# Performance work log

Hardware: AMD Instinct MI355X
Metric: run time of the kernel (lower is better)

The kernel has to match this reference:

```python
import jax, jax.numpy as jnp
import numpy as np

ALPHA = 300.0   # attractor_alpha
N_ATT = 16      # n_attractors
MIN_D = 0.001
MAX_D = 10.0


def _resize_bilinear_ac(x, out_h, out_w):
    """Bilinear resize with align_corners=True on trailing (H, W) dims of [B,C,h,w]."""
    h, w = x.shape[-2], x.shape[-1]
    ys = jnp.arange(out_h, dtype=jnp.float32) * ((h - 1) / max(out_h - 1, 1))
    xs = jnp.arange(out_w, dtype=jnp.float32) * ((w - 1) / max(out_w - 1, 1))
    y0 = jnp.floor(ys).astype(jnp.int32); y1 = jnp.minimum(y0 + 1, h - 1)
    x0 = jnp.floor(xs).astype(jnp.int32); x1 = jnp.minimum(x0 + 1, w - 1)
    wy = (ys - y0.astype(jnp.float32))[:, None]   # [out_h, 1]
    wx = (xs - x0.astype(jnp.float32))[None, :]   # [1, out_w]
    v00 = x[..., y0[:, None], x0[None, :]]
    v01 = x[..., y0[:, None], x1[None, :]]
    v10 = x[..., y1[:, None], x0[None, :]]
    v11 = x[..., y1[:, None], x1[None, :]]
    top = v00 * (1 - wx) + v01 * wx
    bot = v10 * (1 - wx) + v11 * wx
    return top * (1 - wy) + bot * wy


def setup_inputs() -> dict:
    key = jax.random.key(0)
    k = jax.random.split(key, 7)
    B, C, H, W = 4, 128, 192, 192
    n_bins = 64
    x = jax.random.normal(k[0], (B, C, H, W), dtype=jnp.float32)
    prev_bin = jax.random.uniform(k[1], (B, n_bins, H // 2, W // 2), dtype=jnp.float32)
    prev_bin_embedding = jax.random.normal(k[2], (B, C, H // 2, W // 2), dtype=jnp.float32)
    w1 = jax.random.normal(k[3], (128, 128), dtype=jnp.float32) * 0.05
    b1 = jnp.zeros((128,), dtype=jnp.float32)
    w2 = jax.random.normal(k[4], (2 * N_ATT, 128), dtype=jnp.float32) * 0.05
    b2 = jnp.zeros((2 * N_ATT,), dtype=jnp.float32)
    return {"x": x, "prev_bin": prev_bin, "prev_bin_embedding": prev_bin_embedding,
            "w1": w1, "b1": b1, "w2": w2, "b2": b2}


def reference(x, prev_bin, prev_bin_embedding, w1, b1, w2, b2):
    B, C, H, W = x.shape
    # add (interpolated) previous bin embedding
    pe = _resize_bilinear_ac(prev_bin_embedding, H, W)
    h = x + pe
    # per-pixel MLP (two 1x1 convs)
    h = jax.nn.relu(jnp.einsum('bchw,oc->bohw', h, w1) + b1[:, None, None])
    att = jax.nn.relu(jnp.einsum('bchw,oc->bohw', h, w2) + b2[:, None, None]) + 0.001
    # [B, n_attractors, 2, H, W] -> take normed attractor points
    att = att.reshape(B, N_ATT, 2, H, W)[:, :, 0]          # [B, nA, H, W]
    # upsample previous bin centers to feature resolution
    bc = _resize_bilinear_ac(prev_bin, H, W)               # [B, nB, H, W]
    # broadcast-subtract + inverse attractor + mean over attractors
    dx = att[:, :, None, :, :] - bc[:, None, :, :, :]      # [B, nA, nB, H, W]
    delta_c = jnp.mean(dx / (1.0 + ALPHA * dx * dx), axis=1)  # gamma = 2
    bin_new_centers = bc + delta_c
    bin_centers = (MAX_D - MIN_D) * bin_new_centers + MIN_D
    bin_centers = jnp.clip(jnp.sort(bin_centers, axis=1), MIN_D, MAX_D)
    return bin_new_centers, bin_centers
```

## Files before the change

### kernel.cpp

```cpp
#include <hip/hip_runtime.h>

constexpr int Bc = 4, Cc = 128, Hc = 192, Wc = 192;
constexpr int HI = 96, WI = 96;
constexpr int NB = 64;
constexpr int NA = 16;
constexpr float SCL = 95.0f / 191.0f;

typedef __attribute__((ext_vector_type(8))) short bf16x8;
typedef __attribute__((ext_vector_type(4))) float f32x4;

__device__ __forceinline__ unsigned short f2bf(float f) {
  unsigned u = __builtin_bit_cast(unsigned, f);
  unsigned r = (u + 0x7FFFu + ((u >> 16) & 1u)) >> 16;
  return (unsigned short)r;
}

__device__ __forceinline__ float rcp_fast(float r) {
#if defined(__has_builtin)
#if __has_builtin(__builtin_amdgcn_rcpf)
  return __builtin_amdgcn_rcpf(r);
#else
  return 1.0f / r;
#endif
#else
  return 1.0f / r;
#endif
}

__global__ __launch_bounds__(256) void k_prep(
    const float* __restrict__ w1, const float* __restrict__ w2,
    unsigned short* __restrict__ w1bf, unsigned short* __restrict__ w2bf)
{
  const int t = blockIdx.x * 256 + threadIdx.x;
  if (t < 16384) {
    w1bf[t] = f2bf(w1[t]);
  } else {
    const int u = t - 16384;
    const int j = u >> 7, c = u & 127;
    w2bf[u] = f2bf(w2[(2 * j) * 128 + c]);
  }
}

__global__ __launch_bounds__(256) void k_att(
    const float* __restrict__ x, const float* __restrict__ pbe,
    const unsigned short* __restrict__ w1bf, const float* __restrict__ b1,
    const unsigned short* __restrict__ w2bf, const float* __restrict__ b2,
    float* __restrict__ att)
{
  constexpr int PH = 136;
  __shared__ __align__(16) unsigned char smem[64 * PH * 2 + 128 * 36 * 4];
  unsigned short* h_s  = (unsigned short*)smem;
  float*          row_s = (float*)(smem + 64 * PH * 2);
  unsigned short* a1_s = (unsigned short*)(smem + 64 * PH * 2);

  const int tid = threadIdx.x;
  const int xg0 = blockIdx.x * 64;
  const int y = blockIdx.y;
  const int b = blockIdx.z;

  const float ysf = y * SCL;
  const int y0 = (int)ysf;
  const int y1 = min(y0 + 1, HI - 1);
  const float wy = ysf - (float)y0;
  const int xi0 = (int)(xg0 * SCL);

  #pragma unroll
  for (int i = 0; i < 18; ++i) {
    const int f = tid + 256 * i;
    const int c = f / 36;
    const int xi = f - c * 36;
    const int xgl = min(xi0 + xi, WI - 1);
    const float* p = pbe + (size_t)(b * Cc + c) * (HI * WI);
    const float top = p[y0 * WI + xgl];
    const float bot = p[y1 * WI + xgl];
    row_s[c * 36 + xi] = top + wy * (bot - top);
  }
  __syncthreads();

  #pragma unroll
  for (int i = 0; i < 8; ++i) {
    const int f4 = tid + 256 * i;
    const int c = f4 >> 4;
    const int q = f4 & 15;
    const float4 xv = *(const float4*)&x[((size_t)(b * Cc + c) * Hc + y) * Wc + xg0 + 4 * q];
    const float xa[4] = {xv.x, xv.y, xv.z, xv.w};
    #pragma unroll
    for (int r = 0; r < 4; ++r) {
      const int px = 4 * q + r;
      const float xsf = (float)(xg0 + px) * SCL;
      const int x0 = (int)xsf;
      const float wx = xsf - (float)x0;
      const int xl = x0 - xi0;
      const float v0 = row_s[c * 36 + xl];
      const float v1 = row_s[c * 36 + xl + 1];
      h_s[px * PH + c] = f2bf(xa[r] + v0 + wx * (v1 - v0));
    }
  }
  __syncthreads();

  const int lane = tid & 63;
  const int wv = tid >> 6;
  const int ln = lane & 15;
  const int qd = lane >> 4;
  const int m0 = wv * 16;

  bf16x8 af[4];
  #pragma unroll
  for (int kt = 0; kt < 4; ++kt)
    af[kt] = *(const bf16x8*)&h_s[(m0 + ln) * PH + kt * 32 + qd * 8];

  f32x4 acc[8];
  #pragma unroll
  for (int nt = 0; nt < 8; ++nt) acc[nt] = f32x4{0.f, 0.f, 0.f, 0.f};

  #pragma unroll
  for (int nt = 0; nt < 8; ++nt) {
    #pragma unroll
    for (int kt = 0; kt < 4; ++kt) {
      const bf16x8 bf = *(const bf16x8*)&w1bf[(nt * 16 + ln) * 128 + kt * 32 + qd * 8];
      acc[nt] = __builtin_amdgcn_mfma_f32_16x16x32_bf16(af[kt], bf, acc[nt], 0, 0, 0);
    }
  }

  #pragma unroll
  for (int nt = 0; nt < 8; ++nt) {
    const int n = nt * 16 + ln;
    const float bias = b1[n];
    #pragma unroll
    for (int r = 0; r < 4; ++r) {
      const int m = m0 + qd * 4 + r;
      a1_s[m * PH + n] = f2bf(fmaxf(acc[nt][r] + bias, 0.f));
    }
  }

  f32x4 acc2 = f32x4{0.f, 0.f, 0.f, 0.f};
  #pragma unroll
  for (int kt = 0; kt < 4; ++kt) {
    const bf16x8 a2 = *(const bf16x8*)&a1_s[(m0 + ln) * PH + kt * 32 + qd * 8];
    const bf16x8 b2f = *(const bf16x8*)&w2bf[ln * 128 + kt * 32 + qd * 8];
    acc2 = __builtin_amdgcn_mfma_f32_16x16x32_bf16(a2, b2f, acc2, 0, 0, 0);
  }
  const float bias2 = b2[2 * ln];
  #pragma unroll
  for (int r = 0; r < 4; ++r) {
    const int px = m0 + qd * 4 + r;
    const float v = fmaxf(acc2[r] + bias2, 0.f) + 0.001f;
    att[((size_t)((b * Hc + y) * Wc) + xg0 + px) * NA + ln] = v;
  }
}

__global__ __launch_bounds__(192) void k_bins(
    const float* __restrict__ pb, const float* __restrict__ att,
    float* __restrict__ out0, float* __restrict__ out1)
{
  __shared__ __align__(16) float pbs[NB][2][WI];

  const int tid = threadIdx.x;
  const int y = blockIdx.x;
  const int b = blockIdx.y;

  const float ysf = y * SCL;
  const int y0 = (int)ysf;
  const int y1 = min(y0 + 1, HI - 1);
  const float wy = ysf - (float)y0;

  #pragma unroll
  for (int i = 0; i < 16; ++i) {
    const int u = tid + 192 * i;
    const int k = u / 48;
    const int rem = u - k * 48;
    const int r = rem / 24;
    const int xi4 = rem - r * 24;
    const int yr = r ? y1 : y0;
    const float4 v = *(const float4*)&pb[(size_t)(b * NB + k) * (HI * WI) + yr * WI + xi4 * 4];
    *(float4*)&pbs[k][r][xi4 * 4] = v;
  }

  float am[16];
  {
    const float4* ap = (const float4*)(att + ((size_t)((b * Hc + y) * Wc) + tid) * NA);
    const float4 a0 = ap[0], a1 = ap[1], a2 = ap[2], a3 = ap[3];
    am[0] = a0.x;  am[1] = a0.y;  am[2] = a0.z;  am[3] = a0.w;
    am[4] = a1.x;  am[5] = a1.y;  am[6] = a1.z;  am[7] = a1.w;
    am[8] = a2.x;  am[9] = a2.y;  am[10] = a2.z; am[11] = a2.w;
    am[12] = a3.x; am[13] = a3.y; am[14] = a3.z; am[15] = a3.w;
  }
  __syncthreads();

  const float xsf = tid * SCL;
  const int x0 = (int)xsf;
  const float wx = xsf - (float)x0;

  const size_t obase = (size_t)(b * NB) * (Hc * Wc) + (size_t)y * Wc + tid;
  float v[NB];

  #pragma unroll
  for (int k = 0; k < NB; ++k) {
    const float v00 = pbs[k][0][x0], v01 = pbs[k][0][x0 + 1];
    const float v10 = pbs[k][1][x0], v11 = pbs[k][1][x0 + 1];
    const float top = v00 + wx * (v01 - v00);
    const float bot = v10 + wx * (v11 - v10);
    const float bc = top + wy * (bot - top);
    float delta = 0.f;
    #pragma unroll
    for (int j = 0; j < NA; ++j) {
      const float d = am[j] - bc;
      const float rq = fmaf(300.f * d, d, 1.f);
      delta = fmaf(d, rcp_fast(rq), delta);
    }
    const float bnc = fmaf(delta, 1.f / 16.f, bc);
    out0[obase + (size_t)k * (Hc * Wc)] = bnc;
    v[k] = fmaf(9.999f, bnc, 0.001f);
  }

  #pragma unroll
  for (int size = 2; size <= NB; size <<= 1) {
    #pragma unroll
    for (int stride = size >> 1; stride >= 1; stride >>= 1) {
      #pragma unroll
      for (int i = 0; i < NB; ++i) {
        if ((i & stride) == 0) {
          const int j = i | stride;
          const bool asc = ((i & size) == 0);
          const float a = v[i], c = v[j];
          const float lo = fminf(a, c), hi = fmaxf(a, c);
          v[i] = asc ? lo : hi;
          v[j] = asc ? hi : lo;
        }
      }
    }
  }

  #pragma unroll
  for (int k = 0; k < NB; ++k) {
    out1[obase + (size_t)k * (Hc * Wc)] = fminf(fmaxf(v[k], 0.001f), 10.0f);
  }
}

extern "C" void kernel_launch(void* const* d_in, const int* in_sizes, int n_in,
                              void* d_out, int out_size, void* d_ws, size_t ws_size,
                              hipStream_t stream) {
  const float* x   = (const float*)d_in[0];
  const float* pb  = (const float*)d_in[1];
  const float* pbe = (const float*)d_in[2];
  const float* w1  = (const float*)d_in[3];
  const float* b1  = (const float*)d_in[4];
  const float* w2  = (const float*)d_in[5];
  const float* b2  = (const float*)d_in[6];

  float* out0 = (float*)d_out;
  float* out1 = out0 + (size_t)Bc * NB * Hc * Wc;

  unsigned short* w1bf = (unsigned short*)d_ws;
  unsigned short* w2bf = w1bf + 16384;
  float* att = (float*)((char*)d_ws + 65536);

  k_prep<<<72, 256, 0, stream>>>(w1, w2, w1bf, w2bf);

  dim3 g1(Wc / 64, Hc, Bc);
  k_att<<<g1, 256, 0, stream>>>(x, pbe, w1bf, b1, w2bf, b2, att);

  dim3 g2(Hc, Bc);
  k_bins<<<g2, 192, 0, stream>>>(pb, att, out0, out1);
}
```

Baseline: 242.6 us.

## Fuse attractor MLP and bin-center update into one kernel with split bitonic sort

Merges the attractor MLP kernel and the bin-update/sort kernel into a single kernel. Attractor values now stay in shared memory instead of making a round trip through a global workspace. The prev_bin rows are prefetched into registers while the MFMAs run. The 64-element per-pixel sort is split across two threads, each sorting 32 values, followed by a merge step through shared memory. This cuts register pressure and drops one launch, at the cost of more shared memory, extra barriers, and idle threads during the sort.

After: 264.7 us. 1.09x slower.

```diff
diff --git a/kernel.cpp b/kernel.cpp
--- a/kernel.cpp
+++ b/kernel.cpp
@@ -41,17 +41,21 @@
   }
 }
 
-__global__ __launch_bounds__(256) void k_att(
+__global__ __launch_bounds__(256) void k_fused(
     const float* __restrict__ x, const float* __restrict__ pbe,
+    const float* __restrict__ pb,
     const unsigned short* __restrict__ w1bf, const float* __restrict__ b1,
     const unsigned short* __restrict__ w2bf, const float* __restrict__ b2,
-    float* __restrict__ att)
+    float* __restrict__ out0, float* __restrict__ out1)
 {
   constexpr int PH = 136;
-  __shared__ __align__(16) unsigned char smem[64 * PH * 2 + 128 * 36 * 4];
-  unsigned short* h_s  = (unsigned short*)smem;
-  float*          row_s = (float*)(smem + 64 * PH * 2);
-  unsigned short* a1_s = (unsigned short*)(smem + 64 * PH * 2);
+  __shared__ __align__(16) unsigned char smem[40000];
+  unsigned short* h_s   = (unsigned short*)smem;
+  float*          pbs   = (float*)smem;
+  float*          row_s = (float*)(smem + 17408);
+  unsigned short* a1_s  = (unsigned short*)(smem + 17408);
+  float*          srt   = (float*)(smem + 17408);
+  float*          att_s = (float*)(smem + 35840);
 
   const int tid = threadIdx.x;
   const int xg0 = blockIdx.x * 64;
@@ -108,11 +112,24 @@
   #pragma unroll
   for (int kt = 0; kt < 4; ++kt)
     af[kt] = *(const bf16x8*)&h_s[(m0 + ln) * PH + kt * 32 + qd * 8];
+  __syncthreads();
+
+  float pbv[17];
+  #pragma unroll
+  for (int i = 0; i < 17; ++i) {
+    const int u = tid + 256 * i;
+    const int k = u / 68;
+    const int rem = u - k * 68;
+    const int r = (rem >= 34) ? 1 : 0;
+    const int xi = rem - 34 * r;
+    const int xgl = min(xi0 + xi, WI - 1);
+    const int yr = r ? y1 : y0;
+    pbv[i] = pb[(size_t)(b * NB + k) * (HI * WI) + yr * WI + xgl];
+  }
 
   f32x4 acc[8];
   #pragma unroll
   for (int nt = 0; nt < 8; ++nt) acc[nt] = f32x4{0.f, 0.f, 0.f, 0.f};
-
   #pragma unroll
   for (int nt = 0; nt < 8; ++nt) {
     #pragma unroll
@@ -140,100 +157,107 @@
     const bf16x8 b2f = *(const bf16x8*)&w2bf[ln * 128 + kt * 32 + qd * 8];
     acc2 = __builtin_amdgcn_mfma_f32_16x16x32_bf16(a2, b2f, acc2, 0, 0, 0);
   }
-  const float bias2 = b2[2 * ln];
-  #pragma unroll
-  for (int r = 0; r < 4; ++r) {
-    const int px = m0 + qd * 4 + r;
-    const float v = fmaxf(acc2[r] + bias2, 0.f) + 0.001f;
-    att[((size_t)((b * Hc + y) * Wc) + xg0 + px) * NA + ln] = v;
-  }
-}
-
-__global__ __launch_bounds__(192) void k_bins(
-    const float* __restrict__ pb, const float* __restrict__ att,
-    float* __restrict__ out0, float* __restrict__ out1)
-{
-  __shared__ __align__(16) float pbs[NB][2][WI];
-
-  const int tid = threadIdx.x;
-  const int y = blockIdx.x;
-  const int b = blockIdx.y;
-
-  const float ysf = y * SCL;
-  const int y0 = (int)ysf;
-  const int y1 = min(y0 + 1, HI - 1);
-  const float wy = ysf - (float)y0;
-
-  #pragma unroll
-  for (int i = 0; i < 16; ++i) {
-    const int u = tid + 192 * i;
-    const int k = u / 48;
-    const int rem = u - k * 48;
-    const int r = rem / 24;
-    const int xi4 = rem - r * 24;
-    const int yr = r ? y1 : y0;
-    const float4 v = *(const float4*)&pb[(size_t)(b * NB + k) * (HI * WI) + yr * WI + xi4 * 4];
-    *(float4*)&pbs[k][r][xi4 * 4] = v;
-  }
-
-  float am[16];
   {
-    const float4* ap = (const float4*)(att + ((size_t)((b * Hc + y) * Wc) + tid) * NA);
-    const float4 a0 = ap[0], a1 = ap[1], a2 = ap[2], a3 = ap[3];
-    am[0] = a0.x;  am[1] = a0.y;  am[2] = a0.z;  am[3] = a0.w;
-    am[4] = a1.x;  am[5] = a1.y;  am[6] = a1.z;  am[7] = a1.w;
-    am[8] = a2.x;  am[9] = a2.y;  am[10] = a2.z; am[11] = a2.w;
-    am[12] = a3.x; am[13] = a3.y; am[14] = a3.z; am[15] = a3.w;
-  }
-  __syncthreads();
-
-  const float xsf = tid * SCL;
-  const int x0 = (int)xsf;
-  const float wx = xsf - (float)x0;
-
-  const size_t obase = (size_t)(b * NB) * (Hc * Wc) + (size_t)y * Wc + tid;
-  float v[NB];
-
-  #pragma unroll
-  for (int k = 0; k < NB; ++k) {
-    const float v00 = pbs[k][0][x0], v01 = pbs[k][0][x0 + 1];
-    const float v10 = pbs[k][1][x0], v11 = pbs[k][1][x0 + 1];
-    const float top = v00 + wx * (v01 - v00);
-    const float bot = v10 + wx * (v11 - v10);
-    const float bc = top + wy * (bot - top);
-    float delta = 0.f;
-    #pragma unroll
-    for (int j = 0; j < NA; ++j) {
-      const float d = am[j] - bc;
-      const float rq = fmaf(300.f * d, d, 1.f);
-      delta = fmaf(d, rcp_fast(rq), delta);
-    }
-    const float bnc = fmaf(delta, 1.f / 16.f, bc);
-    out0[obase + (size_t)k * (Hc * Wc)] = bnc;
-    v[k] = fmaf(9.999f, bnc, 0.001f);
-  }
-
-  #pragma unroll
-  for (int size = 2; size <= NB; size <<= 1) {
-    #pragma unroll
-    for (int stride = size >> 1; stride >= 1; stride >>= 1) {
+    const float bias2 = b2[2 * ln];
+    #pragma unroll
+    for (int r = 0; r < 4; ++r) {
+      const int px = m0 + qd * 4 + r;
+      att_s[ln * 65 + px] = fmaxf(acc2[r] + bias2, 0.f) + 0.001f;
+    }
+  }
+
+  #pragma unroll
+  for (int i = 0; i < 17; ++i)
+    pbs[tid + 256 * i] = pbv[i];
+  __syncthreads();
+
+  const int px = tid & 63;
+  const int xg = xg0 + px;
+  {
+    const float xsf = xg * SCL;
+    const int x0 = (int)xsf;
+    const float wx = xsf - (float)x0;
+    const int xl = x0 - xi0;
+
+    float am[16];
+    #pragma unroll
+    for (int j = 0; j < NA; ++j) am[j] = att_s[j * 65 + px];
+
+    const size_t obase = (size_t)(b * NB) * (Hc * Wc) + (size_t)y * Wc + xg;
+    #pragma unroll
+    for (int i = 0; i < 16; ++i) {
+      const int k = wv * 16 + i;
+      const float v00 = pbs[k * 68 + xl],      v01 = pbs[k * 68 + xl + 1];
+      const float v10 = pbs[k * 68 + 34 + xl], v11 = pbs[k * 68 + 34 + xl + 1];
+      const float top = v00 + wx * (v01 - v00);
+      const float bot = v10 + wx * (v11 - v10);
+      const float bc = top + wy * (bot - top);
+      float delta = 0.f;
       #pragma unroll
-      for (int i = 0; i < NB; ++i) {
+      for (int j = 0; j < NA; ++j) {
+        const float d = am[j] - bc;
+        const float rq = fmaf(300.f * d, d, 1.f);
+        delta = fmaf(d, rcp_fast(rq), delta);
+      }
+      const float bnc = fmaf(delta, 1.f / 16.f, bc);
+      out0[obase + (size_t)k * (Hc * Wc)] = bnc;
+      srt[k * 64 + px] = fmaf(9.999f, bnc, 0.001f);
+    }
+  }
+  __syncthreads();
+
+  float sv[32];
+  const int half = tid >> 6;
+  if (tid < 128) {
+    #pragma unroll
+    for (int i = 0; i < 32; ++i) sv[i] = srt[(half * 32 + i) * 64 + px];
+    const bool desc = (half == 1);
+    #pragma unroll
+    for (int size = 2; size <= 32; size <<= 1) {
+      #pragma unroll
+      for (int stride = size >> 1; stride >= 1; stride >>= 1) {
+        #pragma unroll
+        for (int i = 0; i < 32; ++i) {
+          if ((i & stride) == 0) {
+            const int j = i | stride;
+            const bool up = (((i & size) == 0) != desc);
+            const float a = sv[i], c = sv[j];
+            const float lo = fminf(a, c), hi = fmaxf(a, c);
+            sv[i] = up ? lo : hi;
+            sv[j] = up ? hi : lo;
+          }
+        }
+      }
+    }
+    #pragma unroll
+    for (int i = 0; i < 32; ++i) srt[(half * 32 + i) * 64 + px] = sv[i];
+  }
+  __syncthreads();
+
+  if (tid < 128) {
+    #pragma unroll
+    for (int i = 0; i < 32; ++i) {
+      const float partner = srt[((1 - half) * 32 + i) * 64 + px];
+      sv[i] = half ? fmaxf(sv[i], partner) : fminf(sv[i], partner);
+    }
+    #pragma unroll
+    for (int stride = 16; stride >= 1; stride >>= 1) {
+      #pragma unroll
+      for (int i = 0; i < 32; ++i) {
         if ((i & stride) == 0) {
           const int j = i | stride;
-          const bool asc = ((i & size) == 0);
-          const float a = v[i], c = v[j];
-          const float lo = fminf(a, c), hi = fmaxf(a, c);
-          v[i] = asc ? lo : hi;
-          v[j] = asc ? hi : lo;
+          const float a = sv[i], c = sv[j];
+          sv[i] = fminf(a, c);
+          sv[j] = fmaxf(a, c);
         }
       }
     }
-  }
-
-  #pragma unroll
-  for (int k = 0; k < NB; ++k) {
-    out1[obase + (size_t)k * (Hc * Wc)] = fminf(fmaxf(v[k], 0.001f), 10.0f);
+    const size_t obase = (size_t)(b * NB) * (Hc * Wc) + (size_t)y * Wc + xg0 + px;
+    #pragma unroll
+    for (int i = 0; i < 32; ++i) {
+      const int k = half * 32 + i;
+      out1[obase + (size_t)k * (Hc * Wc)] = fminf(fmaxf(sv[i], 0.001f), 10.0f);
+    }
   }
 }
 
@@ -253,13 +277,9 @@
 
   unsigned short* w1bf = (unsigned short*)d_ws;
   unsigned short* w2bf = w1bf + 16384;
-  float* att = (float*)((char*)d_ws + 65536);
 
   k_prep<<<72, 256, 0, stream>>>(w1, w2, w1bf, w2bf);
 
-  dim3 g1(Wc / 64, Hc, Bc);
-  k_att<<<g1, 256, 0, stream>>>(x, pbe, w1bf, b1, w2bf, b2, att);
-
-  dim3 g2(Hc, Bc);
-  k_bins<<<g2, 192, 0, stream>>>(pb, att, out0, out1);
-}
+  dim3 grid(Wc / 64, Hc, Bc);
+  k_fused<<<grid, 256, 0, stream>>>(x, pbe, pb, w1bf, b1, w2bf, b2, out0, out1);
+}
```

## Fuse x load and horizontal interp into MFMA fragment build, shrink LDS

Applied to the files above, without the earlier changes.

k_att no longer stages the interpolated activations in a separate LDS tile. Each lane now reads x straight from global memory and interpolates from a bf16 row buffer while building its MFMA A fragments, which drops one LDS round trip and one barrier and shrinks LDS to allow more resident blocks. The cost is uncoalesced scalar global loads of x (one pixel per lane across channels) and bf16 rounding of the interpolated embedding. k_bins interleaves four bins per attractor loop for ILP, and both kernels get occupancy hints in launch_bounds.

New measurement: 242.5 us. No clear change (-0.0%).

```diff
diff --git a/kernel.cpp b/kernel.cpp
--- a/kernel.cpp
+++ b/kernel.cpp
@@ -14,7 +14,10 @@
   unsigned r = (u + 0x7FFFu + ((u >> 16) & 1u)) >> 16;
   return (unsigned short)r;
 }
-
+__device__ __forceinline__ float bf2f(unsigned short h) {
+  unsigned u = ((unsigned)h) << 16;
+  return __builtin_bit_cast(float, u);
+}
 __device__ __forceinline__ float rcp_fast(float r) {
 #if defined(__has_builtin)
 #if __has_builtin(__builtin_amdgcn_rcpf)
@@ -41,17 +44,16 @@
   }
 }
 
-__global__ __launch_bounds__(256) void k_att(
+__global__ __launch_bounds__(256, 4) void k_att(
     const float* __restrict__ x, const float* __restrict__ pbe,
     const unsigned short* __restrict__ w1bf, const float* __restrict__ b1,
     const unsigned short* __restrict__ w2bf, const float* __restrict__ b2,
     float* __restrict__ att)
 {
   constexpr int PH = 136;
-  __shared__ __align__(16) unsigned char smem[64 * PH * 2 + 128 * 36 * 4];
-  unsigned short* h_s  = (unsigned short*)smem;
-  float*          row_s = (float*)(smem + 64 * PH * 2);
-  unsigned short* a1_s = (unsigned short*)(smem + 64 * PH * 2);
+  __shared__ __align__(16) unsigned char smem[64 * PH * 2];
+  unsigned short* rowb = (unsigned short*)smem;
+  unsigned short* a1_s = (unsigned short*)smem;
 
   const int tid = threadIdx.x;
   const int xg0 = blockIdx.x * 64;
@@ -73,28 +75,7 @@
     const float* p = pbe + (size_t)(b * Cc + c) * (HI * WI);
     const float top = p[y0 * WI + xgl];
     const float bot = p[y1 * WI + xgl];
-    row_s[c * 36 + xi] = top + wy * (bot - top);
-  }
-  __syncthreads();
-
-  #pragma unroll
-  for (int i = 0; i < 8; ++i) {
-    const int f4 = tid + 256 * i;
-    const int c = f4 >> 4;
-    const int q = f4 & 15;
-    const float4 xv = *(const float4*)&x[((size_t)(b * Cc + c) * Hc + y) * Wc + xg0 + 4 * q];
-    const float xa[4] = {xv.x, xv.y, xv.z, xv.w};
-    #pragma unroll
-    for (int r = 0; r < 4; ++r) {
-      const int px = 4 * q + r;
-      const float xsf = (float)(xg0 + px) * SCL;
-      const int x0 = (int)xsf;
-      const float wx = xsf - (float)x0;
-      const int xl = x0 - xi0;
-      const float v0 = row_s[c * 36 + xl];
-      const float v1 = row_s[c * 36 + xl + 1];
-      h_s[px * PH + c] = f2bf(xa[r] + v0 + wx * (v1 - v0));
-    }
+    rowb[c * 36 + xi] = f2bf(top + wy * (bot - top));
   }
   __syncthreads();
 
@@ -104,15 +85,30 @@
   const int qd = lane >> 4;
   const int m0 = wv * 16;
 
+  const int px = m0 + ln;
+  const int xg = xg0 + px;
+  const float xsf = (float)xg * SCL;
+  const int x0i = (int)xsf;
+  const float wx = xsf - (float)x0i;
+  const int xl = x0i - xi0;
+
   bf16x8 af[4];
   #pragma unroll
-  for (int kt = 0; kt < 4; ++kt)
-    af[kt] = *(const bf16x8*)&h_s[(m0 + ln) * PH + kt * 32 + qd * 8];
+  for (int kt = 0; kt < 4; ++kt) {
+    #pragma unroll
+    for (int j = 0; j < 8; ++j) {
+      const int c = kt * 32 + qd * 8 + j;
+      const float xv = x[((size_t)(b * Cc + c) * Hc + y) * Wc + xg];
+      const float v0 = bf2f(rowb[c * 36 + xl]);
+      const float v1 = bf2f(rowb[c * 36 + xl + 1]);
+      af[kt][j] = (short)f2bf(xv + v0 + wx * (v1 - v0));
+    }
+  }
+  __syncthreads();
 
   f32x4 acc[8];
   #pragma unroll
   for (int nt = 0; nt < 8; ++nt) acc[nt] = f32x4{0.f, 0.f, 0.f, 0.f};
-
   #pragma unroll
   for (int nt = 0; nt < 8; ++nt) {
     #pragma unroll
@@ -143,13 +139,13 @@
   const float bias2 = b2[2 * ln];
   #pragma unroll
   for (int r = 0; r < 4; ++r) {
-    const int px = m0 + qd * 4 + r;
+    const int opx = m0 + qd * 4 + r;
     const float v = fmaxf(acc2[r] + bias2, 0.f) + 0.001f;
-    att[((size_t)((b * Hc + y) * Wc) + xg0 + px) * NA + ln] = v;
-  }
-}
-
-__global__ __launch_bounds__(192) void k_bins(
+    att[((size_t)((b * Hc + y) * Wc) + xg0 + opx) * NA + ln] = v;
+  }
+}
+
+__global__ __launch_bounds__(192, 2) void k_bins(
     const float* __restrict__ pb, const float* __restrict__ att,
     float* __restrict__ out0, float* __restrict__ out1)
 {
@@ -195,22 +191,34 @@
   float v[NB];
 
   #pragma unroll
-  for (int k = 0; k < NB; ++k) {
-    const float v00 = pbs[k][0][x0], v01 = pbs[k][0][x0 + 1];
-    const float v10 = pbs[k][1][x0], v11 = pbs[k][1][x0 + 1];
-    const float top = v00 + wx * (v01 - v00);
-    const float bot = v10 + wx * (v11 - v10);
-    const float bc = top + wy * (bot - top);
-    float delta = 0.f;
+  for (int kb = 0; kb < NB; kb += 4) {
+    float bc[4], dl[4];
+    #pragma unroll
+    for (int q = 0; q < 4; ++q) {
+      const int k = kb + q;
+      const float v00 = pbs[k][0][x0], v01 = pbs[k][0][x0 + 1];
+      const float v10 = pbs[k][1][x0], v11 = pbs[k][1][x0 + 1];
+      const float top = v00 + wx * (v01 - v00);
+      const float bot = v10 + wx * (v11 - v10);
+      bc[q] = top + wy * (bot - top);
+      dl[q] = 0.f;
+    }
     #pragma unroll
     for (int j = 0; j < NA; ++j) {
-      const float d = am[j] - bc;
-      const float rq = fmaf(300.f * d, d, 1.f);
-      delta = fmaf(d, rcp_fast(rq), delta);
-    }
-    const float bnc = fmaf(delta, 1.f / 16.f, bc);
-    out0[obase + (size_t)k * (Hc * Wc)] = bnc;
-    v[k] = fmaf(9.999f, bnc, 0.001f);
+      const float a = am[j];
+      #pragma unroll
+      for (int q = 0; q < 4; ++q) {
+        const float d = a - bc[q];
+        const float rq = fmaf(300.f * d, d, 1.f);
+        dl[q] = fmaf(d, rcp_fast(rq), dl[q]);
+      }
+    }
+    #pragma unroll
+    for (int q = 0; q < 4; ++q) {
+      const float bnc = fmaf(dl[q], 1.f / 16.f, bc[q]);
+      out0[obase + (size_t)(kb + q) * (Hc * Wc)] = bnc;
+      v[kb + q] = fmaf(9.999f, bnc, 0.001f);
+    }
   }
 
   #pragma unroll
```
